# Performance work log

Hardware: AMD Instinct MI355X
Metric: run time of the kernel (lower is better)

The kernel has to match this reference:

```python
import jax, jax.numpy as jnp
import numpy as np

E = 64          # num_experts
TOPK = 8        # num_experts_per_tok
I = 512         # moe_intermediate_size
H = 1024        # hidden_size
G = 128         # awq group_size
T = 2048        # tokens (batch*seq)

# AWQ nibble unpack order: bit shifts [0,16,4,20,8,24,12,28] -> indices [0,4,1,5,2,6,3,7]
_AWQ_SHIFTS = jnp.array([0, 4, 1, 5, 2, 6, 3, 7], dtype=jnp.int32) * 4


def awq_dequant(qw, qz, scales, group_size=G):
    """qw: (K, N//8) int32, qz: (K//G, N//8) int32, scales: (K//G, N) float.
    Returns dense weight (K, N): (q - z) * scale with per-group zero/scale."""
    K = qw.shape[0]
    uq = ((qw[:, :, None] >> _AWQ_SHIFTS) & 0xF).reshape(K, -1)          # (K, N)
    uz = ((qz[:, :, None] >> _AWQ_SHIFTS) & 0xF).reshape(qz.shape[0], -1)  # (K//G, N)
    uz = jnp.repeat(uz, group_size, axis=0)                               # (K, N)
    sc = jnp.repeat(scales, group_size, axis=0)                           # (K, N)
    return (uq.astype(scales.dtype) - uz.astype(scales.dtype)) * sc


def setup_inputs() -> dict:
    key = jax.random.key(0)
    ks = jax.random.split(key, 8)
    imax = 2**31 - 1
    return {
        "x": jax.random.normal(ks[0], (T, H), dtype=jnp.float32),
        "gate_w": jax.random.normal(ks[1], (E, H), dtype=jnp.float32) * 0.02,
        "qweight1": jax.random.randint(ks[2], (H, (E * I) // 8), 0, imax, dtype=jnp.int32),
        "qzeros1": jax.random.randint(ks[3], (H // G, (E * I) // 8), 0, imax, dtype=jnp.int32),
        "scales1": jax.random.normal(ks[4], (H // G, E * I), dtype=jnp.float32) * 0.02,
        "qweight2": jax.random.randint(ks[5], (I, (E * H) // 8), 0, imax, dtype=jnp.int32),
        "qzeros2": jax.random.randint(ks[6], (I // G, (E * H) // 8), 0, imax, dtype=jnp.int32),
        "scales2": jax.random.normal(ks[7], (I // G, E * H), dtype=jnp.float32) * 0.02,
    }


def reference(x, gate_w, qweight1, qzeros1, scales1, qweight2, qzeros2, scales2):
    # dequant grouped expert weights
    w1 = awq_dequant(qweight1, qzeros1, scales1).T.reshape(E, I, H)   # (E, I, H)
    w2 = awq_dequant(qweight2, qzeros2, scales2).T.reshape(E, H, I)   # (E, H, I)

    # routing: softmax -> top-k -> renormalize
    logits = x @ gate_w.T                                             # (T, E)
    probs = jax.nn.softmax(logits, axis=-1)
    topv, topi = jax.lax.top_k(probs, TOPK)                           # (T, K)
    topv = topv / jnp.sum(topv, axis=-1, keepdims=True)
    cw = jnp.sum(jax.nn.one_hot(topi, E, dtype=x.dtype) * topv[..., None], axis=1)  # (T, E)

    # experts: out = sum_e cw[t,e] * silu(x @ w1[e].T) @ w2[e].T
    h = jax.nn.silu(jnp.einsum('th,eih->tei', x, w1))                 # (T, E, I)
    h = h * cw[:, :, None]                                            # fold combine weights
    out = jnp.einsum('tei,ehi->th', h, w2)                            # (T, H)
    return out
```

## Files before the change

kernel.cpp:

```cpp
#include <hip/hip_runtime.h>
#include <hip/hip_bf16.h>

#define T_TOK 2048
#define HID   1024
#define EXP   64
#define TOPK  8
#define IMED  512
#define N1 (EXP * IMED)
#define C1 (N1 / 8)
#define N2 (EXP * HID)
#define C2 (N2 / 8)
#define MAXTILES 320

typedef _Float16 h16x2 __attribute__((ext_vector_type(2)));
typedef _Float16 h16x8 __attribute__((ext_vector_type(8)));
typedef float f32x4 __attribute__((ext_vector_type(4)));
typedef unsigned short ushortx4 __attribute__((ext_vector_type(4)));
typedef unsigned short ushortx8 __attribute__((ext_vector_type(8)));

__constant__ int kShifts[8] = {0, 16, 4, 20, 8, 24, 12, 28};

__device__ __forceinline__ void async16(const void* g, void* l) {
  __builtin_amdgcn_global_load_lds((const __attribute__((address_space(1))) void*)g,
                                   (__attribute__((address_space(3))) void*)l, 16, 0, 0);
}

__device__ __forceinline__ unsigned short f2h(float f) {
  return __builtin_bit_cast(unsigned short, (_Float16)f);
}
__device__ __forceinline__ float h2f(unsigned short b) {
  return (float)__builtin_bit_cast(_Float16, b);
}

__device__ __forceinline__ h16x8 unpack8h(unsigned q, h16x2 sh2, h16x2 zh2) {
  union { unsigned u[4]; h16x8 v; } out;
#pragma unroll
  for (int j = 0; j < 4; ++j) {
    const unsigned m = ((q >> (4 * j)) & 0x000F000Fu) | 0x64006400u;
    h16x2 d = __builtin_bit_cast(h16x2, m) - zh2;
    d = d * sh2;
    out.u[j] = __builtin_bit_cast(unsigned, d);
  }
  return out.v;
}

__global__ __launch_bounds__(256) void cast_x_kernel(const float* __restrict__ x,
                                                     unsigned short* __restrict__ xh) {
  const int i = (blockIdx.x * 256 + threadIdx.x) * 4;
  float4 v = *reinterpret_cast<const float4*>(x + i);
  ushortx4 o;
  o[0] = f2h(v.x); o[1] = f2h(v.y); o[2] = f2h(v.z); o[3] = f2h(v.w);
  *reinterpret_cast<ushortx4*>(xh + i) = o;
}

__global__ __launch_bounds__(256) void logits_f32_kernel(
    const float* __restrict__ x, const float* __restrict__ gate_w,
    float* __restrict__ partial) {
  const int t0 = blockIdx.x * 64;
  const int k0 = blockIdx.y * 128;
  const int tid = threadIdx.x;

  __shared__ float xs[64][128];
  __shared__ float gs[64][128];

  const int lrow = tid >> 5;
  const int cblk = tid & 31;
#pragma unroll
  for (int r = 0; r < 8; ++r) {
    const int row = r * 8 + lrow;
    const int sc = (cblk ^ ((row >> 2) & 7)) * 4;
    float4 xv = *reinterpret_cast<const float4*>(x + (size_t)(t0 + row) * HID + k0 + cblk * 4);
    float4 gv = *reinterpret_cast<const float4*>(gate_w + (size_t)row * HID + k0 + cblk * 4);
    *reinterpret_cast<float4*>(&xs[row][sc]) = xv;
    *reinterpret_cast<float4*>(&gs[row][sc]) = gv;
  }
  __syncthreads();

  const int tg = (tid >> 4) * 4;
  const int eg = (tid & 15) * 4;
  const int xsw = (tid >> 4) & 7;
  const int gsw = tid & 7;
  float acc[4][4] = {{0.f}};
#pragma unroll 8
  for (int k = 0; k < 128; k += 4) {
    const int c = k >> 2;
    float4 a[4], b[4];
#pragma unroll
    for (int i = 0; i < 4; ++i)
      a[i] = *reinterpret_cast<const float4*>(&xs[tg + i][(c ^ xsw) * 4]);
#pragma unroll
    for (int j = 0; j < 4; ++j)
      b[j] = *reinterpret_cast<const float4*>(&gs[eg + j][(c ^ gsw) * 4]);
#pragma unroll
    for (int i = 0; i < 4; ++i)
#pragma unroll
      for (int j = 0; j < 4; ++j) {
        acc[i][j] = fmaf(a[i].x, b[j].x, acc[i][j]);
        acc[i][j] = fmaf(a[i].y, b[j].y, acc[i][j]);
        acc[i][j] = fmaf(a[i].z, b[j].z, acc[i][j]);
        acc[i][j] = fmaf(a[i].w, b[j].w, acc[i][j]);
      }
  }
  float* dst = partial + ((size_t)blockIdx.y * T_TOK + t0) * EXP;
#pragma unroll
  for (int i = 0; i < 4; ++i)
    *reinterpret_cast<float4*>(dst + (tg + i) * EXP + eg) =
        make_float4(acc[i][0], acc[i][1], acc[i][2], acc[i][3]);
}

__global__ __launch_bounds__(256) void topk_kernel(
    const float* __restrict__ partial, int* __restrict__ counts,
    int* __restrict__ tok_list, int* __restrict__ hslot_list,
    float* __restrict__ cw_list) {
  const int wave = threadIdx.x >> 6, lane = threadIdx.x & 63;
  const int t = blockIdx.x * 4 + wave;
  float lg = 0.f;
#pragma unroll
  for (int s = 0; s < 8; ++s)
    lg += partial[((size_t)s * T_TOK + t) * EXP + lane];

  float m = lg;
  for (int off = 32; off; off >>= 1) m = fmaxf(m, __shfl_xor(m, off));
  float pe = expf(lg - m);
  float s = pe;
  for (int off = 32; off; off >>= 1) s += __shfl_xor(s, off);
  float prob = pe / s;

  float pcur = prob;
  float myv = 0.f;
  int myi = -1;
  float tsum = 0.f;
  for (int k = 0; k < TOPK; ++k) {
    float vv = pcur;
    int idx = lane;
    for (int off = 32; off; off >>= 1) {
      float ov = __shfl_xor(vv, off);
      int oi = __shfl_xor(idx, off);
      if (ov > vv || (ov == vv && oi < idx)) { vv = ov; idx = oi; }
    }
    tsum += vv;
    if (lane == k) { myv = vv; myi = idx; }
    if (lane == idx) pcur = -1.f;
  }

  if (lane < TOPK) {
    const float cw = myv / tsum;
    const int ex = myi;
    const int slot = atomicAdd(&counts[ex], 1);
    tok_list[ex * T_TOK + slot] = t;
    hslot_list[ex * T_TOK + slot] = t * TOPK + lane;
    cw_list[ex * T_TOK + slot] = cw;
  }
}

__global__ __launch_bounds__(64) void build_tiles_kernel(
    const int* __restrict__ counts, int2* __restrict__ tiles, int* __restrict__ tile_cnt) {
  const int lane = threadIdx.x;
  const int n = counts[lane];
  const int nt = (n + 63) >> 6;
  int off = nt;
  for (int d = 1; d < 64; d <<= 1) {
    const int v = __shfl_up(off, d);
    if (lane >= d) off += v;
  }
  const int excl = off - nt;
  for (int i = 0; i < nt; ++i) tiles[excl + i] = make_int2(lane, i * 64);
  if (lane == 63) *tile_cnt = excl + nt;
}

__global__ __launch_bounds__(256) void repack_kernel(
    const int* __restrict__ qw, unsigned* __restrict__ qk, int K, int C) {
  const int pp = blockIdx.y;
  const int t = pp >> 2, fq = pp & 3;
  const int c2 = blockIdx.x * 512 + threadIdx.x * 2;
  const int nblk = c2 >> 1;
  unsigned o0[16], o1[16];
#pragma unroll
  for (int i = 0; i < 16; ++i) { o0[i] = 0u; o1[i] = 0u; }
  const int k0a = t * 64 + fq * 8;
  const int k0b = t * 64 + (fq + 4) * 8;
#pragma unroll
  for (int r = 0; r < 8; ++r) {
    const int2 va = *reinterpret_cast<const int2*>(qw + (size_t)(k0a + r) * C + c2);
    const int2 vb = *reinterpret_cast<const int2*>(qw + (size_t)(k0b + r) * C + c2);
    const int outsh = (r & 1) * 16 + (r >> 1) * 4;
    const unsigned qa[2] = {(unsigned)va.x, (unsigned)va.y};
    const unsigned qb[2] = {(unsigned)vb.x, (unsigned)vb.y};
#pragma unroll
    for (int ci = 0; ci < 2; ++ci) {
#pragma unroll
      for (int j = 0; j < 8; ++j) {
        const int sh = kShifts[j];
        o0[ci * 8 + j] |= ((qa[ci] >> sh) & 0xFu) << outsh;
        o1[ci * 8 + j] |= ((qb[ci] >> sh) & 0xFu) << outsh;
      }
    }
  }
  unsigned* dst = qk + (size_t)nblk * 2 * K + t * 128 + fq * 32;
#pragma unroll
  for (int idx = 0; idx < 16; ++idx)
    *reinterpret_cast<uint2*>(dst + idx * 2) = make_uint2(o0[idx], o1[idx]);
}

__global__ __launch_bounds__(256) void mfma_gemm1(
    const unsigned short* __restrict__ xh, const unsigned* __restrict__ qk1,
    const int* __restrict__ qz1, const float* __restrict__ sc1,
    const int* __restrict__ counts, const int2* __restrict__ tiles,
    const int* __restrict__ tile_cnt, const int* __restrict__ tok_list,
    const int* __restrict__ hslot_list, const float* __restrict__ cw_list,
    unsigned short* __restrict__ h_buf) {
  if ((int)blockIdx.y >= *tile_cnt) return;
  const int2 te = tiles[blockIdx.y];
  const int e = te.x;
  const int t0 = te.y;
  const int n_e = counts[e];
  const int ntile = blockIdx.x;
  const int tid = threadIdx.x;
  const int wave = tid >> 6, lane = tid & 63;
  const int fr = lane & 15, fq = lane >> 4;

  __shared__ unsigned short As[2][64 * 64];

  const int arow = tid >> 3;
  const int acb = ((tid & 7) ^ ((tid >> 3) & 7)) * 16;
  const int ta0 = tok_list[e * T_TOK + min(t0 + arow, n_e - 1)];
  const int ta1 = tok_list[e * T_TOK + min(t0 + 32 + arow, n_e - 1)];
  const char* ga0 = (const char*)(xh + (size_t)ta0 * HID) + acb;
  const char* ga1 = (const char*)(xh + (size_t)ta1 * HID) + acb;

  auto stage = [&](int b) {
    char* l = (char*)&As[b][0] + wave * 1024;
    async16(ga0, l);
    async16(ga1, l + 4096);
    ga0 += 128; ga1 += 128;
  };

  const int nbase = e * IMED + ntile * 64 + wave * 16;
  const unsigned* bp = qk1 + (size_t)(nbase >> 4) * (2 * HID) + fq * 32 + fr * 2;
  const int col = nbase + fr;
  const int shz = ((fr >> 1) & 3) * 4 + (fr & 1) * 16;

  f32x4 acc[4];
#pragma unroll
  for (int i = 0; i < 4; ++i) acc[i] = (f32x4){0.f, 0.f, 0.f, 0.f};

  stage(0);
  uint2 qcur = *reinterpret_cast<const uint2*>(bp);
  float s_cur = sc1[col];
  unsigned zd_cur = (unsigned)qz1[col >> 3];
  int p = 0;
#pragma unroll 1
  for (int g = 0; g < HID / 128; ++g) {
    const unsigned shb = (unsigned)f2h(s_cur);
    const h16x2 sh2 = __builtin_bit_cast(h16x2, shb | (shb << 16));
    const unsigned zb = 0x6400u | ((zd_cur >> shz) & 15u);
    const h16x2 zh2 = __builtin_bit_cast(h16x2, zb | (zb << 16));
    float s_nxt = 0.f; unsigned zd_nxt = 0u;
#pragma unroll
    for (int hh = 0; hh < 2; ++hh) {
      const int t = g * 2 + hh;
      __syncthreads();
      if (t + 1 < HID / 64) stage(p ^ 1);
      uint2 qnext = make_uint2(0u, 0u);
      if (t + 1 < HID / 64) qnext = *reinterpret_cast<const uint2*>(bp + (t + 1) * 128);
      if (hh == 1 && g + 1 < HID / 128) {
        s_nxt = sc1[(size_t)(g + 1) * N1 + col];
        zd_nxt = (unsigned)qz1[(size_t)(g + 1) * C1 + (col >> 3)];
      }
      const h16x8 b0 = unpack8h(qcur.x, sh2, zh2);
      const h16x8 b1 = unpack8h(qcur.y, sh2, zh2);
#pragma unroll
      for (int kk = 0; kk < 2; ++kk) {
        const h16x8 bb = kk ? b1 : b0;
#pragma unroll
        for (int i = 0; i < 4; ++i) {
          const int row = i * 16 + fr;
          const h16x8 a = *reinterpret_cast<const h16x8*>(
              &As[p][row * 64 + (((kk * 4 + fq) ^ (fr & 7)) * 8)]);
          acc[i] = __builtin_amdgcn_mfma_f32_16x16x32_f16(a, bb, acc[i], 0, 0, 0);
        }
      }
      qcur = qnext; p ^= 1;
    }
    s_cur = s_nxt; zd_cur = zd_nxt;
  }

#pragma unroll
  for (int i = 0; i < 4; ++i) {
#pragma unroll
    for (int r = 0; r < 4; ++r) {
      const int grow = t0 + i * 16 + fq * 4 + r;
      if (grow < n_e) {
        const float cw = cw_list[e * T_TOK + grow];
        const int hs = hslot_list[e * T_TOK + grow];
        const float v = acc[i][r];
        h_buf[(size_t)hs * IMED + ntile * 64 + wave * 16 + fr] =
            f2h((v / (1.f + expf(-v))) * cw);
      }
    }
  }
}

__global__ __launch_bounds__(256) void mfma_gemm2(
    const unsigned short* __restrict__ h_buf, const unsigned* __restrict__ qk2,
    const int* __restrict__ qz2, const float* __restrict__ sc2,
    const int* __restrict__ counts, const int2* __restrict__ tiles,
    const int* __restrict__ tile_cnt, const int* __restrict__ hslot_list,
    unsigned short* __restrict__ p_buf) {
  if ((int)blockIdx.y >= *tile_cnt) return;
  const int2 te = tiles[blockIdx.y];
  const int e = te.x;
  const int t0 = te.y;
  const int n_e = counts[e];
  const int ntile = blockIdx.x;
  const int tid = threadIdx.x;
  const int wave = tid >> 6, lane = tid & 63;
  const int fr = lane & 15, fq = lane >> 4;

  __shared__ unsigned short As[2][64 * 64];

  const int arow = tid >> 3;
  const int acb = ((tid & 7) ^ ((tid >> 3) & 7)) * 16;
  const int ha0 = hslot_list[e * T_TOK + min(t0 + arow, n_e - 1)];
  const int ha1 = hslot_list[e * T_TOK + min(t0 + 32 + arow, n_e - 1)];
  const char* ga0 = (const char*)(h_buf + (size_t)ha0 * IMED) + acb;
  const char* ga1 = (const char*)(h_buf + (size_t)ha1 * IMED) + acb;

  auto stage = [&](int b) {
    char* l = (char*)&As[b][0] + wave * 1024;
    async16(ga0, l);
    async16(ga1, l + 4096);
    ga0 += 128; ga1 += 128;
  };

  const int nbase = e * HID + ntile * 64 + wave * 16;
  const unsigned* bp = qk2 + (size_t)(nbase >> 4) * (2 * IMED) + fq * 32 + fr * 2;
  const int col = nbase + fr;
  const int shz = ((fr >> 1) & 3) * 4 + (fr & 1) * 16;

  f32x4 acc[4];
#pragma unroll
  for (int i = 0; i < 4; ++i) acc[i] = (f32x4){0.f, 0.f, 0.f, 0.f};

  stage(0);
  uint2 qcur = *reinterpret_cast<const uint2*>(bp);
  float s_cur = sc2[col];
  unsigned zd_cur = (unsigned)qz2[col >> 3];
  int p = 0;
#pragma unroll 1
  for (int g = 0; g < IMED / 128; ++g) {
    const unsigned shb = (unsigned)f2h(s_cur);
    const h16x2 sh2 = __builtin_bit_cast(h16x2, shb | (shb << 16));
    const unsigned zb = 0x6400u | ((zd_cur >> shz) & 15u);
    const h16x2 zh2 = __builtin_bit_cast(h16x2, zb | (zb << 16));
    float s_nxt = 0.f; unsigned zd_nxt = 0u;
#pragma unroll
    for (int hh = 0; hh < 2; ++hh) {
      const int t = g * 2 + hh;
      __syncthreads();
      if (t + 1 < IMED / 64) stage(p ^ 1);
      uint2 qnext = make_uint2(0u, 0u);
      if (t + 1 < IMED / 64) qnext = *reinterpret_cast<const uint2*>(bp + (t + 1) * 128);
      if (hh == 1 && g + 1 < IMED / 128) {
        s_nxt = sc2[(size_t)(g + 1) * N2 + col];
        zd_nxt = (unsigned)qz2[(size_t)(g + 1) * C2 + (col >> 3)];
      }
      const h16x8 b0 = unpack8h(qcur.x, sh2, zh2);
      const h16x8 b1 = unpack8h(qcur.y, sh2, zh2);
#pragma unroll
      for (int kk = 0; kk < 2; ++kk) {
        const h16x8 bb = kk ? b1 : b0;
#pragma unroll
        for (int i = 0; i < 4; ++i) {
          const int row = i * 16 + fr;
          const h16x8 a = *reinterpret_cast<const h16x8*>(
              &As[p][row * 64 + (((kk * 4 + fq) ^ (fr & 7)) * 8)]);
          acc[i] = __builtin_amdgcn_mfma_f32_16x16x32_f16(a, bb, acc[i], 0, 0, 0);
        }
      }
      qcur = qnext; p ^= 1;
    }
    s_cur = s_nxt; zd_cur = zd_nxt;
  }

#pragma unroll
  for (int i = 0; i < 4; ++i) {
#pragma unroll
    for (int r = 0; r < 4; ++r) {
      const int grow = t0 + i * 16 + fq * 4 + r;
      if (grow < n_e) {
        const int hs = hslot_list[e * T_TOK + grow];
        p_buf[(size_t)hs * HID + ntile * 64 + wave * 16 + fr] = f2h(acc[i][r]);
      }
    }
  }
}

__global__ __launch_bounds__(256) void reduce_kernel(const unsigned short* __restrict__ p_buf,
                                                     float* __restrict__ out) {
  const int idx = blockIdx.x * 256 + threadIdx.x;
  const int t = idx >> 7;
  const int c0 = (idx & 127) * 8;
  float s[8] = {0.f, 0.f, 0.f, 0.f, 0.f, 0.f, 0.f, 0.f};
#pragma unroll
  for (int k = 0; k < TOPK; ++k) {
    ushortx8 v = *reinterpret_cast<const ushortx8*>(p_buf + ((size_t)t * TOPK + k) * HID + c0);
#pragma unroll
    for (int j = 0; j < 8; ++j) s[j] += h2f(v[j]);
  }
  float* dst = out + (size_t)t * HID + c0;
  *reinterpret_cast<float4*>(dst) = make_float4(s[0], s[1], s[2], s[3]);
  *reinterpret_cast<float4*>(dst + 4) = make_float4(s[4], s[5], s[6], s[7]);
}

extern "C" void kernel_launch(void* const* d_in, const int* in_sizes, int n_in,
                              void* d_out, int out_size, void* d_ws, size_t ws_size,
                              hipStream_t stream) {
  const float* x      = (const float*)d_in[0];
  const float* gate_w = (const float*)d_in[1];
  const int*   qw1    = (const int*)d_in[2];
  const int*   qz1    = (const int*)d_in[3];
  const float* sc1    = (const float*)d_in[4];
  const int*   qw2    = (const int*)d_in[5];
  const int*   qz2    = (const int*)d_in[6];
  const float* sc2    = (const float*)d_in[7];
  float* out = (float*)d_out;

  char* ws = (char*)d_ws;
  int* counts           = (int*)(ws);
  int* tok_list         = (int*)(ws + 256);
  int* hslot_list       = (int*)(ws + 524544);
  float* cw_list        = (float*)(ws + 1048832);
  unsigned short* h_buf = (unsigned short*)(ws + 1573120);
  unsigned short* xh    = (unsigned short*)(ws + 18350336);
  unsigned* qk1         = (unsigned*)(ws + 22544640);
  unsigned* qk2         = (unsigned*)(ws + 39321856);
  unsigned short* p_buf = (unsigned short*)(ws + 56099072);
  float* partial        = (float*)(ws + 89653504);
  int2* tiles           = (int2*)(ws + 93847552);
  int* tile_cnt         = (int*)(ws + 93851648);

  hipMemsetAsync(counts, 0, 256, stream);

  cast_x_kernel<<<(T_TOK * HID / 4) / 256, 256, 0, stream>>>(x, xh);
  logits_f32_kernel<<<dim3(T_TOK / 64, HID / 128), 256, 0, stream>>>(x, gate_w, partial);
  topk_kernel<<<T_TOK / 4, 256, 0, stream>>>(partial, counts, tok_list, hslot_list, cw_list);
  build_tiles_kernel<<<1, 64, 0, stream>>>(counts, tiles, tile_cnt);
  repack_kernel<<<dim3(C1 / 512, HID / 16), 256, 0, stream>>>(qw1, qk1, HID, C1);
  repack_kernel<<<dim3(C2 / 512, IMED / 16), 256, 0, stream>>>(qw2, qk2, IMED, C2);

  mfma_gemm1<<<dim3(IMED / 64, MAXTILES), 256, 0, stream>>>(
      xh, qk1, qz1, sc1, counts, tiles, tile_cnt, tok_list, hslot_list, cw_list, h_buf);
  mfma_gemm2<<<dim3(HID / 64, MAXTILES), 256, 0, stream>>>(
      h_buf, qk2, qz2, sc2, counts, tiles, tile_cnt, hslot_list, p_buf);
  reduce_kernel<<<(T_TOK * HID / 8) / 256, 256, 0, stream>>>(p_buf, out);
}
```

Measured before the change: 251.8 us.

## Fuse cast, logits, and weight repacks into one prep kernel; fold tile build into topk

Merges the x-to-fp16 cast, the gate-logit partial GEMM (now split into 16 K-slices of 64), and both weight repack passes into a single heterogeneous prep kernel dispatched by block index. The cast reuses the x loads already made for the logits. The counts memset moves into this kernel, and the tile-list build moves into the last-finishing topk block through an atomic ticket. This removes several launches and the memset, and lets the logit and repack work run concurrently. In exchange it adds a threadfence/atomic completion pattern, reuses the p_buf region for the partials, and reads a partial buffer twice as large in topk.

```diff
diff --git a/kernel.cpp b/kernel.cpp
--- a/kernel.cpp
+++ b/kernel.cpp
@@ -44,79 +44,119 @@
   return out.v;
 }
 
-__global__ __launch_bounds__(256) void cast_x_kernel(const float* __restrict__ x,
-                                                     unsigned short* __restrict__ xh) {
-  const int i = (blockIdx.x * 256 + threadIdx.x) * 4;
-  float4 v = *reinterpret_cast<const float4*>(x + i);
-  ushortx4 o;
-  o[0] = f2h(v.x); o[1] = f2h(v.y); o[2] = f2h(v.z); o[3] = f2h(v.w);
-  *reinterpret_cast<ushortx4*>(xh + i) = o;
-}
-
-__global__ __launch_bounds__(256) void logits_f32_kernel(
+__device__ __forceinline__ void repack_body(const int* __restrict__ qw,
+                                            unsigned* __restrict__ qk, int K, int C,
+                                            int gx, int pp, int tid) {
+  const int t = pp >> 2, fq = pp & 3;
+  const int c2 = gx * 512 + tid * 2;
+  const int nblk = c2 >> 1;
+  unsigned o0[16], o1[16];
+#pragma unroll
+  for (int i = 0; i < 16; ++i) { o0[i] = 0u; o1[i] = 0u; }
+  const int k0a = t * 64 + fq * 8;
+  const int k0b = t * 64 + (fq + 4) * 8;
+#pragma unroll
+  for (int r = 0; r < 8; ++r) {
+    const int2 va = *reinterpret_cast<const int2*>(qw + (size_t)(k0a + r) * C + c2);
+    const int2 vb = *reinterpret_cast<const int2*>(qw + (size_t)(k0b + r) * C + c2);
+    const int outsh = (r & 1) * 16 + (r >> 1) * 4;
+    const unsigned qa[2] = {(unsigned)va.x, (unsigned)va.y};
+    const unsigned qb[2] = {(unsigned)vb.x, (unsigned)vb.y};
+#pragma unroll
+    for (int ci = 0; ci < 2; ++ci) {
+#pragma unroll
+      for (int j = 0; j < 8; ++j) {
+        const int sh = kShifts[j];
+        o0[ci * 8 + j] |= ((qa[ci] >> sh) & 0xFu) << outsh;
+        o1[ci * 8 + j] |= ((qb[ci] >> sh) & 0xFu) << outsh;
+      }
+    }
+  }
+  unsigned* dst = qk + (size_t)nblk * 2 * K + t * 128 + fq * 32;
+#pragma unroll
+  for (int idx = 0; idx < 16; ++idx)
+    *reinterpret_cast<uint2*>(dst + idx * 2) = make_uint2(o0[idx], o1[idx]);
+}
+
+__global__ __launch_bounds__(256) void prep_kernel(
     const float* __restrict__ x, const float* __restrict__ gate_w,
-    float* __restrict__ partial) {
-  const int t0 = blockIdx.x * 64;
-  const int k0 = blockIdx.y * 128;
+    unsigned short* __restrict__ xh, float* __restrict__ partial,
+    const int* __restrict__ qw1, unsigned* __restrict__ qk1,
+    const int* __restrict__ qw2, unsigned* __restrict__ qk2,
+    int* __restrict__ counts, int* __restrict__ done_ctr) {
+  const int bid = blockIdx.x;
   const int tid = threadIdx.x;
-
-  __shared__ float xs[64][128];
-  __shared__ float gs[64][128];
-
-  const int lrow = tid >> 5;
-  const int cblk = tid & 31;
-#pragma unroll
-  for (int r = 0; r < 8; ++r) {
-    const int row = r * 8 + lrow;
-    const int sc = (cblk ^ ((row >> 2) & 7)) * 4;
-    float4 xv = *reinterpret_cast<const float4*>(x + (size_t)(t0 + row) * HID + k0 + cblk * 4);
-    float4 gv = *reinterpret_cast<const float4*>(gate_w + (size_t)row * HID + k0 + cblk * 4);
-    *reinterpret_cast<float4*>(&xs[row][sc]) = xv;
-    *reinterpret_cast<float4*>(&gs[row][sc]) = gv;
-  }
-  __syncthreads();
-
-  const int tg = (tid >> 4) * 4;
-  const int eg = (tid & 15) * 4;
-  const int xsw = (tid >> 4) & 7;
-  const int gsw = tid & 7;
-  float acc[4][4] = {{0.f}};
-#pragma unroll 8
-  for (int k = 0; k < 128; k += 4) {
-    const int c = k >> 2;
-    float4 a[4], b[4];
+  if (bid == 1535) {
+    if (tid < 64) counts[tid] = 0;
+    if (tid == 64) *done_ctr = 0;
+  }
+  if (bid < 512) {
+    __shared__ float xs[64][64];
+    __shared__ float gs[64][64];
+    const int t0 = (bid & 31) * 64;
+    const int ks = bid >> 5;
+    const int k0 = ks * 64;
+    const int lrow = tid >> 4;
+    const int cblk = tid & 15;
+#pragma unroll
+    for (int r = 0; r < 4; ++r) {
+      const int row = r * 16 + lrow;
+      const int sc = (cblk ^ ((row >> 2) & 15)) * 4;
+      float4 xv = *reinterpret_cast<const float4*>(x + (size_t)(t0 + row) * HID + k0 + cblk * 4);
+      float4 gv = *reinterpret_cast<const float4*>(gate_w + (size_t)row * HID + k0 + cblk * 4);
+      *reinterpret_cast<float4*>(&xs[row][sc]) = xv;
+      *reinterpret_cast<float4*>(&gs[row][sc]) = gv;
+      ushortx4 o;
+      o[0] = f2h(xv.x); o[1] = f2h(xv.y); o[2] = f2h(xv.z); o[3] = f2h(xv.w);
+      *reinterpret_cast<ushortx4*>(xh + (size_t)(t0 + row) * HID + k0 + cblk * 4) = o;
+    }
+    __syncthreads();
+    const int tg = (tid >> 4) * 4, eg = (tid & 15) * 4;
+    const int xsw = tid >> 4, gsw = tid & 15;
+    float acc[4][4] = {{0.f, 0.f, 0.f, 0.f}};
+#pragma unroll 4
+    for (int c = 0; c < 16; ++c) {
+      float4 a[4], b[4];
+#pragma unroll
+      for (int i = 0; i < 4; ++i)
+        a[i] = *reinterpret_cast<const float4*>(&xs[tg + i][(c ^ xsw) * 4]);
+#pragma unroll
+      for (int j = 0; j < 4; ++j)
+        b[j] = *reinterpret_cast<const float4*>(&gs[eg + j][(c ^ gsw) * 4]);
+#pragma unroll
+      for (int i = 0; i < 4; ++i)
+#pragma unroll
+        for (int j = 0; j < 4; ++j) {
+          acc[i][j] = fmaf(a[i].x, b[j].x, acc[i][j]);
+          acc[i][j] = fmaf(a[i].y, b[j].y, acc[i][j]);
+          acc[i][j] = fmaf(a[i].z, b[j].z, acc[i][j]);
+          acc[i][j] = fmaf(a[i].w, b[j].w, acc[i][j]);
+        }
+    }
+    float* dst = partial + ((size_t)ks * T_TOK + t0) * EXP;
 #pragma unroll
     for (int i = 0; i < 4; ++i)
-      a[i] = *reinterpret_cast<const float4*>(&xs[tg + i][(c ^ xsw) * 4]);
-#pragma unroll
-    for (int j = 0; j < 4; ++j)
-      b[j] = *reinterpret_cast<const float4*>(&gs[eg + j][(c ^ gsw) * 4]);
-#pragma unroll
-    for (int i = 0; i < 4; ++i)
-#pragma unroll
-      for (int j = 0; j < 4; ++j) {
-        acc[i][j] = fmaf(a[i].x, b[j].x, acc[i][j]);
-        acc[i][j] = fmaf(a[i].y, b[j].y, acc[i][j]);
-        acc[i][j] = fmaf(a[i].z, b[j].z, acc[i][j]);
-        acc[i][j] = fmaf(a[i].w, b[j].w, acc[i][j]);
-      }
-  }
-  float* dst = partial + ((size_t)blockIdx.y * T_TOK + t0) * EXP;
-#pragma unroll
-  for (int i = 0; i < 4; ++i)
-    *reinterpret_cast<float4*>(dst + (tg + i) * EXP + eg) =
-        make_float4(acc[i][0], acc[i][1], acc[i][2], acc[i][3]);
+      *reinterpret_cast<float4*>(dst + (tg + i) * EXP + eg) =
+          make_float4(acc[i][0], acc[i][1], acc[i][2], acc[i][3]);
+  } else if (bid < 1024) {
+    const int id = bid - 512;
+    repack_body(qw1, qk1, HID, C1, id & 7, id >> 3, tid);
+  } else {
+    const int id = bid - 1024;
+    repack_body(qw2, qk2, IMED, C2, id & 15, id >> 4, tid);
+  }
 }
 
 __global__ __launch_bounds__(256) void topk_kernel(
     const float* __restrict__ partial, int* __restrict__ counts,
     int* __restrict__ tok_list, int* __restrict__ hslot_list,
-    float* __restrict__ cw_list) {
+    float* __restrict__ cw_list, int2* __restrict__ tiles,
+    int* __restrict__ tile_cnt, int* __restrict__ done_ctr) {
   const int wave = threadIdx.x >> 6, lane = threadIdx.x & 63;
   const int t = blockIdx.x * 4 + wave;
   float lg = 0.f;
 #pragma unroll
-  for (int s = 0; s < 8; ++s)
+  for (int s = 0; s < 16; ++s)
     lg += partial[((size_t)s * T_TOK + t) * EXP + lane];
 
   float m = lg;
@@ -151,55 +191,25 @@
     hslot_list[ex * T_TOK + slot] = t * TOPK + lane;
     cw_list[ex * T_TOK + slot] = cw;
   }
-}
-
-__global__ __launch_bounds__(64) void build_tiles_kernel(
-    const int* __restrict__ counts, int2* __restrict__ tiles, int* __restrict__ tile_cnt) {
-  const int lane = threadIdx.x;
-  const int n = counts[lane];
-  const int nt = (n + 63) >> 6;
-  int off = nt;
-  for (int d = 1; d < 64; d <<= 1) {
-    const int v = __shfl_up(off, d);
-    if (lane >= d) off += v;
-  }
-  const int excl = off - nt;
-  for (int i = 0; i < nt; ++i) tiles[excl + i] = make_int2(lane, i * 64);
-  if (lane == 63) *tile_cnt = excl + nt;
-}
-
-__global__ __launch_bounds__(256) void repack_kernel(
-    const int* __restrict__ qw, unsigned* __restrict__ qk, int K, int C) {
-  const int pp = blockIdx.y;
-  const int t = pp >> 2, fq = pp & 3;
-  const int c2 = blockIdx.x * 512 + threadIdx.x * 2;
-  const int nblk = c2 >> 1;
-  unsigned o0[16], o1[16];
-#pragma unroll
-  for (int i = 0; i < 16; ++i) { o0[i] = 0u; o1[i] = 0u; }
-  const int k0a = t * 64 + fq * 8;
-  const int k0b = t * 64 + (fq + 4) * 8;
-#pragma unroll
-  for (int r = 0; r < 8; ++r) {
-    const int2 va = *reinterpret_cast<const int2*>(qw + (size_t)(k0a + r) * C + c2);
-    const int2 vb = *reinterpret_cast<const int2*>(qw + (size_t)(k0b + r) * C + c2);
-    const int outsh = (r & 1) * 16 + (r >> 1) * 4;
-    const unsigned qa[2] = {(unsigned)va.x, (unsigned)va.y};
-    const unsigned qb[2] = {(unsigned)vb.x, (unsigned)vb.y};
-#pragma unroll
-    for (int ci = 0; ci < 2; ++ci) {
-#pragma unroll
-      for (int j = 0; j < 8; ++j) {
-        const int sh = kShifts[j];
-        o0[ci * 8 + j] |= ((qa[ci] >> sh) & 0xFu) << outsh;
-        o1[ci * 8 + j] |= ((qb[ci] >> sh) & 0xFu) << outsh;
-      }
-    }
-  }
-  unsigned* dst = qk + (size_t)nblk * 2 * K + t * 128 + fq * 32;
-#pragma unroll
-  for (int idx = 0; idx < 16; ++idx)
-    *reinterpret_cast<uint2*>(dst + idx * 2) = make_uint2(o0[idx], o1[idx]);
+
+  __threadfence();
+  __syncthreads();
+  __shared__ int ticket;
+  if (threadIdx.x == 0) ticket = atomicAdd(done_ctr, 1);
+  __syncthreads();
+  if (ticket == (int)gridDim.x - 1 && threadIdx.x < 64) {
+    const int ln = threadIdx.x;
+    const int n = atomicAdd(&counts[ln], 0);
+    const int nt = (n + 63) >> 6;
+    int off = nt;
+    for (int d = 1; d < 64; d <<= 1) {
+      const int v = __shfl_up(off, d);
+      if (ln >= d) off += v;
+    }
+    const int excl = off - nt;
+    for (int i = 0; i < nt; ++i) tiles[excl + i] = make_int2(ln, i * 64);
+    if (ln == 63) *tile_cnt = excl + nt;
+  }
 }
 
 __global__ __launch_bounds__(256) void mfma_gemm1(
@@ -436,18 +446,15 @@
   unsigned* qk1         = (unsigned*)(ws + 22544640);
   unsigned* qk2         = (unsigned*)(ws + 39321856);
   unsigned short* p_buf = (unsigned short*)(ws + 56099072);
-  float* partial        = (float*)(ws + 89653504);
-  int2* tiles           = (int2*)(ws + 93847552);
-  int* tile_cnt         = (int*)(ws + 93851648);
-
-  hipMemsetAsync(counts, 0, 256, stream);
-
-  cast_x_kernel<<<(T_TOK * HID / 4) / 256, 256, 0, stream>>>(x, xh);
-  logits_f32_kernel<<<dim3(T_TOK / 64, HID / 128), 256, 0, stream>>>(x, gate_w, partial);
-  topk_kernel<<<T_TOK / 4, 256, 0, stream>>>(partial, counts, tok_list, hslot_list, cw_list);
-  build_tiles_kernel<<<1, 64, 0, stream>>>(counts, tiles, tile_cnt);
-  repack_kernel<<<dim3(C1 / 512, HID / 16), 256, 0, stream>>>(qw1, qk1, HID, C1);
-  repack_kernel<<<dim3(C2 / 512, IMED / 16), 256, 0, stream>>>(qw2, qk2, IMED, C2);
+  float* partial        = (float*)(ws + 56099072);
+  int2* tiles           = (int2*)(ws + 89653504);
+  int* tile_cnt         = (int*)(ws + 89656064);
+  int* done_ctr         = (int*)(ws + 89656068);
+
+  prep_kernel<<<1536, 256, 0, stream>>>(x, gate_w, xh, partial, qw1, qk1, qw2, qk2,
+                                        counts, done_ctr);
+  topk_kernel<<<T_TOK / 4, 256, 0, stream>>>(partial, counts, tok_list, hslot_list, cw_list,
+                                             tiles, tile_cnt, done_ctr);
 
   mfma_gemm1<<<dim3(IMED / 64, MAXTILES), 256, 0, stream>>>(
       xh, qk1, qz1, sc1, counts, tiles, tile_cnt, tok_list, hslot_list, cw_list, h_buf);
```

Result: slower. 292.1 us (+16.0%).
